# Kernel optimization log

Hardware: AMD Instinct MI355X
Metric: run time of the kernel (lower is better)

## Reference

```python
import jax, jax.numpy as jnp
import numpy as np
import math

B, T, C = 8, 1024, 1024
H = 16
D = C // H
TI = 256
FF = 4 * C
EPS = 1e-5


def _ln(x, g, b):
    mu = jnp.mean(x, axis=-1, keepdims=True)
    var = jnp.mean(jnp.square(x - mu), axis=-1, keepdims=True)
    return (x - mu) * jax.lax.rsqrt(var + EPS) * g + b


def _gelu_tanh(x):
    return jax.nn.gelu(x, approximate=True)


def setup_inputs() -> dict:
    key = jax.random.key(0)
    ks = jax.random.split(key, 16)
    s = 0.02
    inp = {
        'x': jax.random.normal(ks[0], (B, T, C), jnp.float32),
        'x_img_feats': jax.random.normal(ks[1], (B, TI, C), jnp.float32),
        'ln1_g': jnp.ones((C,), jnp.float32), 'ln1_b': jnp.zeros((C,), jnp.float32),
        'ln2_g': jnp.ones((C,), jnp.float32), 'ln2_b': jnp.zeros((C,), jnp.float32),
        'W_attn': jax.random.normal(ks[2], (C, 3 * C), jnp.float32) * s,
        'b_attn': jnp.zeros((3 * C,), jnp.float32),
        'W_aproj': jax.random.normal(ks[3], (C, C), jnp.float32) * s,
        'b_aproj': jnp.zeros((C,), jnp.float32),
        'Wq': jax.random.normal(ks[4], (C, C), jnp.float32) * s,
        'bq': jnp.zeros((C,), jnp.float32),
        'Wk': jax.random.normal(ks[5], (C, C), jnp.float32) * s,
        'bk': jnp.zeros((C,), jnp.float32),
        'Wv': jax.random.normal(ks[6], (C, C), jnp.float32) * s,
        'bv': jnp.zeros((C,), jnp.float32),
        'Wcproj': jax.random.normal(ks[7], (C, C), jnp.float32) * s,
        'bcproj': jnp.zeros((C,), jnp.float32),
        'W_fc': jax.random.normal(ks[8], (C, FF), jnp.float32) * s,
        'b_fc': jnp.zeros((FF,), jnp.float32),
        'W_mproj': jax.random.normal(ks[9], (FF, C), jnp.float32) * s,
        'b_mproj': jnp.zeros((C,), jnp.float32),
    }
    return inp


def _heads(t):
    # (B, S, C) -> (B, H, S, D)
    return t.reshape(t.shape[0], t.shape[1], H, D).transpose(0, 2, 1, 3)


def _merge(t):
    # (B, H, S, D) -> (B, S, C)
    return t.transpose(0, 2, 1, 3).reshape(t.shape[0], t.shape[2], C)


def reference(x, x_img_feats, ln1_g, ln1_b, ln2_g, ln2_b,
              W_attn, b_attn, W_aproj, b_aproj,
              Wq, bq, Wk, bk, Wv, bv, Wcproj, bcproj,
              W_fc, b_fc, W_mproj, b_mproj):
    scale = 1.0 / math.sqrt(D)

    # causal self-attention
    h = _ln(x, ln1_g, ln1_b)
    qkv = h @ W_attn + b_attn
    q, k, v = jnp.split(qkv, 3, axis=-1)
    q, k, v = _heads(q), _heads(k), _heads(v)
    att = jnp.einsum('bhtd,bhsd->bhts', q, k) * scale
    causal = jnp.tril(jnp.ones((T, T), bool))
    att = jnp.where(causal[None, None], att, -jnp.inf)
    att = jax.nn.softmax(att, axis=-1)
    sa = _merge(jnp.einsum('bhts,bhsd->bhtd', att, v)) @ W_aproj + b_aproj
    x = x + sa

    # cross-attention (text queries, image keys/values)
    ht = _ln(x, ln1_g, ln1_b)
    q = _heads(ht @ Wq + bq)
    k = _heads(x_img_feats @ Wk + bk)
    v = _heads(x_img_feats @ Wv + bv)
    catt = jax.nn.softmax(jnp.einsum('bhtd,bhsd->bhts', q, k) * scale, axis=-1)
    ca = _merge(jnp.einsum('bhts,bhsd->bhtd', catt, v)) @ Wcproj + bcproj
    x = x + ca

    # MLP
    h2 = _ln(x, ln2_g, ln2_b)
    x = x + _gelu_tanh(h2 @ W_fc + b_fc) @ W_mproj + b_mproj
    return x
```

## Files before the change

kernel.cpp:

```cpp
#include <hip/hip_runtime.h>

#define B_ 8
#define T_ 1024
#define C_ 1024
#define H_ 16
#define D_ 64
#define TI_ 256
#define FF_ 4096
#define BT_ (B_*T_)
#define BTI_ (B_*TI_)

typedef __bf16 bf16x8 __attribute__((ext_vector_type(8)));
typedef float f32x4 __attribute__((ext_vector_type(4)));

__device__ __forceinline__ unsigned short f2bf(float f){
  unsigned u = __float_as_uint(f);
  u += 0x7fffu + ((u>>16)&1u);
  return (unsigned short)(u>>16);
}

__device__ __forceinline__ void cp16(const void* g, void* l){
  __builtin_amdgcn_global_load_lds(
      (const __attribute__((address_space(1))) unsigned int*)(unsigned long long)g,
      (__attribute__((address_space(3))) unsigned int*)(unsigned long long)l,
      16, 0, 0);
}

__global__ __launch_bounds__(256) void gemm_bt(
    const unsigned short* __restrict__ A,
    const unsigned short* __restrict__ Bt,
    const float* __restrict__ bias,
    const float* __restrict__ resid,
    void* __restrict__ outp,
    int M, int N, int K, int mode)
{
  __shared__ unsigned short sA[128*64];
  __shared__ unsigned short sB[128*64];
  const int tid  = threadIdx.x;
  const int wid  = tid >> 6;
  const int lane = tid & 63;
  const int quad = lane >> 4;
  const int l16  = lane & 15;
  const int row0 = blockIdx.y * 128;
  const int col0 = blockIdx.x * 128;
  const int wr = (wid >> 1) * 64;
  const int wc = (wid & 1) * 64;

  f32x4 zero = {0.f,0.f,0.f,0.f};
  f32x4 acc[4][4];
#pragma unroll
  for (int i=0;i<4;i++)
#pragma unroll
    for (int j=0;j<4;j++) acc[i][j] = zero;

  for (int k0 = 0; k0 < K; k0 += 64){
    if (k0) __syncthreads();
#pragma unroll
    for (int r=0;r<8;r++){
      int chunk = wid*8 + r;
      int cA = chunk & 15;
      int slot = cA*64 + lane;
      int row = slot >> 3;
      int cc = (slot & 7) ^ (row & 7);
      if (chunk < 16)
        cp16(A  + (size_t)(row0+row)*K + (k0 + cc*8), sA + cA*512);
      else
        cp16(Bt + (size_t)(col0+row)*K + (k0 + cc*8), sB + cA*512);
    }
    __syncthreads();
    const char* sAb = (const char*)sA;
    const char* sBb = (const char*)sB;
#pragma unroll
    for (int kk=0;kk<2;kk++){
      bf16x8 af[4], bfb[4];
#pragma unroll
      for (int i=0;i<4;i++){
        int rr = wr + i*16 + l16;
        af[i] = *(const bf16x8*)(sAb + rr*128 + (((kk*4+quad) ^ (rr&7))<<4));
      }
#pragma unroll
      for (int j=0;j<4;j++){
        int rr = wc + j*16 + l16;
        bfb[j] = *(const bf16x8*)(sBb + rr*128 + (((kk*4+quad) ^ (rr&7))<<4));
      }
#pragma unroll
      for (int i=0;i<4;i++)
#pragma unroll
        for (int j=0;j<4;j++)
          acc[i][j] = __builtin_amdgcn_mfma_f32_16x16x32_bf16(af[i], bfb[j], acc[i][j], 0, 0, 0);
    }
  }

#pragma unroll
  for (int j=0;j<4;j++){
    int gc = col0 + wc + j*16 + l16;
    float bz = bias[gc];
#pragma unroll
    for (int i=0;i<4;i++){
      int gr0 = row0 + wr + i*16 + quad*4;
#pragma unroll
      for (int r=0;r<4;r++){
        float v = acc[i][j][r] + bz;
        size_t idx = (size_t)(gr0+r)*N + gc;
        if (mode == 0){
          ((unsigned short*)outp)[idx] = f2bf(v);
        } else if (mode == 1){
          float t = tanhf(0.7978845608028654f*(v + 0.044715f*v*v*v));
          ((unsigned short*)outp)[idx] = f2bf(0.5f*v*(1.f+t));
        } else {
          ((float*)outp)[idx] = resid[idx] + v;
        }
      }
    }
  }
}

__global__ __launch_bounds__(256) void ln_fwd(
    const float* __restrict__ x, const float* __restrict__ g,
    const float* __restrict__ b, unsigned short* __restrict__ out)
{
  int row = blockIdx.x, t = threadIdx.x;
  const float4* xv = (const float4*)(x + (size_t)row*C_);
  float4 v = xv[t];
  float s  = v.x+v.y+v.z+v.w;
  float ss = v.x*v.x + v.y*v.y + v.z*v.z + v.w*v.w;
#pragma unroll
  for (int o=32;o>0;o>>=1){ s += __shfl_down(s,o); ss += __shfl_down(ss,o); }
  __shared__ float red[16];
  int wid = t>>6, lane = t&63;
  if (lane==0){ red[wid]=s; red[8+wid]=ss; }
  __syncthreads();
  if (t==0){
    red[0] = red[0]+red[1]+red[2]+red[3];
    red[8] = red[8]+red[9]+red[10]+red[11];
  }
  __syncthreads();
  float mu  = red[0] * (1.f/C_);
  float var = red[8] * (1.f/C_) - mu*mu;
  float rstd = rsqrtf(var + 1e-5f);
  float4 gv = ((const float4*)g)[t];
  float4 bv = ((const float4*)b)[t];
  ushort4 o;
  o.x = f2bf((v.x-mu)*rstd*gv.x + bv.x);
  o.y = f2bf((v.y-mu)*rstd*gv.y + bv.y);
  o.z = f2bf((v.z-mu)*rstd*gv.z + bv.z);
  o.w = f2bf((v.w-mu)*rstd*gv.w + bv.w);
  ((ushort4*)(out + (size_t)row*C_))[t] = o;
}

__global__ void wconv_t(const float* __restrict__ W, unsigned short* __restrict__ Wt,
                        int Kd, int Nd)
{
  __shared__ float tile[32][33];
  int tx = threadIdx.x, ty = threadIdx.y;
  int n0 = blockIdx.x*32, k0 = blockIdx.y*32;
#pragma unroll
  for (int j=0;j<4;j++)
    tile[ty+8*j][tx] = W[(size_t)(k0+ty+8*j)*Nd + (n0+tx)];
  __syncthreads();
#pragma unroll
  for (int j=0;j<4;j++)
    Wt[(size_t)(n0+ty+8*j)*Kd + (k0+tx)] = f2bf(tile[tx][ty+8*j]);
}

__global__ void conv_bf16(const float* __restrict__ X, unsigned short* __restrict__ Y, int n4)
{
  int i = blockIdx.x*256 + threadIdx.x;
  if (i < n4){
    float4 v = ((const float4*)X)[i];
    ushort4 o; o.x=f2bf(v.x); o.y=f2bf(v.y); o.z=f2bf(v.z); o.w=f2bf(v.w);
    ((ushort4*)Y)[i] = o;
  }
}

__global__ __launch_bounds__(256) void attn_fwd(
    const unsigned short* __restrict__ Q, int ldq,
    const unsigned short* __restrict__ Kp, const unsigned short* __restrict__ Vp, int ldkv,
    int kvT, int Skv, int Tq, int causal,
    unsigned short* __restrict__ Out, int ldo, float scale)
{
  __shared__ unsigned short sK[64*64];
  __shared__ unsigned short sV[64*64];
  __shared__ unsigned short sP[4*16*64];
  const int tid = threadIdx.x;
  const int wid = tid >> 6;
  const int lane = tid & 63;
  const int quad = lane >> 4;
  const int l16 = lane & 15;
  const int qt = blockIdx.x, h = blockIdx.y, b = blockIdx.z;
  const int hoff = h * D_;

  const int qrow = qt*64 + wid*16 + l16;
  const unsigned short* qb = Q + (size_t)(b*Tq + qrow)*ldq + hoff;
  bf16x8 qf[2];
  qf[0] = *(const bf16x8*)(qb + quad*8);
  qf[1] = *(const bf16x8*)(qb + 32 + quad*8);

  f32x4 zero = {0.f,0.f,0.f,0.f};
  f32x4 O[4];
#pragma unroll
  for (int j=0;j<4;j++) O[j] = zero;
  float mrun[4], lrun[4];
#pragma unroll
  for (int r=0;r<4;r++){ mrun[r] = -1e30f; lrun[r] = 0.f; }

  const int nkb = causal ? (qt+1) : ((Skv+63)>>6);
  char* sPw = (char*)sP + wid*2048;

  for (int kb=0; kb<nkb; ++kb){
    if (kb) __syncthreads();
#pragma unroll
    for (int ss=0; ss<2; ++ss){
      int slot = tid + ss*256;
      int srow = slot >> 3;
      int cc = (slot & 7) ^ (srow & 7);
      const unsigned short* g = Kp + (size_t)(b*kvT + kb*64 + srow)*ldkv + hoff + cc*8;
      *(uint4*)((char*)sK + slot*16) = *(const uint4*)g;
    }
    {
      int s_ = lane;
      int dbase = wid*16;
      const unsigned short* gv = Vp + (size_t)(b*kvT + kb*64 + s_)*ldkv + hoff + dbase;
      unsigned short vals[16];
      *(uint4*)(vals)   = *(const uint4*)(gv);
      *(uint4*)(vals+8) = *(const uint4*)(gv+8);
      int chunk = s_ >> 3;
      int sb = (s_ & 7)*2;
#pragma unroll
      for (int jj=0; jj<16; ++jj){
        int d = dbase + jj;
        *(unsigned short*)((char*)sV + d*128 + ((chunk ^ (d&7))<<4) + sb) = vals[jj];
      }
    }
    __syncthreads();

    f32x4 sacc[4];
#pragma unroll
    for (int j=0;j<4;j++) sacc[j] = zero;
#pragma unroll
    for (int j=0;j<4;j++){
      int krow = j*16 + l16;
#pragma unroll
      for (int kk=0;kk<2;kk++){
        bf16x8 kf = *(const bf16x8*)((const char*)sK + krow*128 + (((kk*4+quad) ^ (krow&7))<<4));
        sacc[j] = __builtin_amdgcn_mfma_f32_16x16x32_bf16(qf[kk], kf, sacc[j], 0, 0, 0);
      }
    }
    const int qa0 = qt*64 + wid*16 + quad*4;
    float sc[4][4];
#pragma unroll
    for (int j=0;j<4;j++){
      int key = kb*64 + j*16 + l16;
#pragma unroll
      for (int r=0;r<4;r++){
        float v = sacc[j][r] * scale;
        if (causal && key > qa0 + r) v = -1e30f;
        sc[j][r] = v;
      }
    }
    float mnew[4], alpha[4], rs[4];
#pragma unroll
    for (int r=0;r<4;r++){
      float m = fmaxf(fmaxf(sc[0][r], sc[1][r]), fmaxf(sc[2][r], sc[3][r]));
#pragma unroll
      for (int msk=1; msk<16; msk<<=1) m = fmaxf(m, __shfl_xor(m, msk));
      mnew[r] = fmaxf(mrun[r], m);
      alpha[r] = __expf(mrun[r] - mnew[r]);
      mrun[r] = mnew[r];
      rs[r] = 0.f;
    }
#pragma unroll
    for (int j=0;j<4;j++){
#pragma unroll
      for (int r=0;r<4;r++){
        float p = __expf(sc[j][r] - mnew[r]);
        rs[r] += p;
        int prow = quad*4 + r;
        int cole = j*16 + l16;
        *(unsigned short*)(sPw + prow*128 + (((cole>>3) ^ (prow&7))<<4) + (cole&7)*2) = f2bf(p);
      }
    }
#pragma unroll
    for (int r=0;r<4;r++){
#pragma unroll
      for (int msk=1; msk<16; msk<<=1) rs[r] += __shfl_xor(rs[r], msk);
      lrun[r] = lrun[r]*alpha[r] + rs[r];
    }
#pragma unroll
    for (int j=0;j<4;j++){
      O[j][0] *= alpha[0]; O[j][1] *= alpha[1];
      O[j][2] *= alpha[2]; O[j][3] *= alpha[3];
    }
    bf16x8 pf[2];
#pragma unroll
    for (int kk=0;kk<2;kk++)
      pf[kk] = *(const bf16x8*)(sPw + l16*128 + (((kk*4+quad) ^ (l16&7))<<4));
#pragma unroll
    for (int j=0;j<4;j++){
      int vrow = j*16 + l16;
#pragma unroll
      for (int kk=0;kk<2;kk++){
        bf16x8 vf = *(const bf16x8*)((const char*)sV + vrow*128 + (((kk*4+quad) ^ (vrow&7))<<4));
        O[j] = __builtin_amdgcn_mfma_f32_16x16x32_bf16(pf[kk], vf, O[j], 0, 0, 0);
      }
    }
  }
#pragma unroll
  for (int j=0;j<4;j++){
#pragma unroll
    for (int r=0;r<4;r++){
      int qa = qt*64 + wid*16 + quad*4 + r;
      float o = O[j][r] / lrun[r];
      Out[(size_t)(b*Tq + qa)*ldo + hoff + j*16 + l16] = f2bf(o);
    }
  }
}

extern "C" void kernel_launch(void* const* d_in, const int* in_sizes, int n_in,
                              void* d_out, int out_size, void* d_ws, size_t ws_size,
                              hipStream_t stream)
{
  const float* x       = (const float*)d_in[0];
  const float* ximg    = (const float*)d_in[1];
  const float* ln1_g   = (const float*)d_in[2];
  const float* ln1_b   = (const float*)d_in[3];
  const float* ln2_g   = (const float*)d_in[4];
  const float* ln2_b   = (const float*)d_in[5];
  const float* W_attn  = (const float*)d_in[6];
  const float* b_attn  = (const float*)d_in[7];
  const float* W_aproj = (const float*)d_in[8];
  const float* b_aproj = (const float*)d_in[9];
  const float* Wq = (const float*)d_in[10];
  const float* bq = (const float*)d_in[11];
  const float* Wk = (const float*)d_in[12];
  const float* bk = (const float*)d_in[13];
  const float* Wv = (const float*)d_in[14];
  const float* bv = (const float*)d_in[15];
  const float* Wcproj  = (const float*)d_in[16];
  const float* bcproj  = (const float*)d_in[17];
  const float* W_fc    = (const float*)d_in[18];
  const float* b_fc    = (const float*)d_in[19];
  const float* W_mproj = (const float*)d_in[20];
  const float* b_mproj = (const float*)d_in[21];

  char* ws = (char*)d_ws;
  unsigned short* wt_attn  = (unsigned short*)(ws + 0);
  unsigned short* wt_aproj = (unsigned short*)(ws + 6291456);
  unsigned short* wt_q     = (unsigned short*)(ws + 8388608);
  unsigned short* wt_k     = (unsigned short*)(ws + 10485760);
  unsigned short* wt_v     = (unsigned short*)(ws + 12582912);
  unsigned short* wt_cproj = (unsigned short*)(ws + 14680064);
  unsigned short* wt_fc    = (unsigned short*)(ws + 16777216);
  unsigned short* wt_mproj = (unsigned short*)(ws + 25165824);
  unsigned short* ximg_bf  = (unsigned short*)(ws + 33554432);
  float*          xcur     = (float*)(ws + 37748736);
  unsigned short* h_bf     = (unsigned short*)(ws + 71303168);
  unsigned short* qkv      = (unsigned short*)(ws + 88080384);
  unsigned short* att_out  = (unsigned short*)(ws + 88080384 + 50331648);
  unsigned short* u_bf     = (unsigned short*)(ws + 88080384);
  unsigned short* q2 = (unsigned short*)(ws + 155189248);
  unsigned short* k2 = (unsigned short*)(ws + 171966464);
  unsigned short* v2 = (unsigned short*)(ws + 176160768);
  unsigned short* ca = (unsigned short*)(ws + 180355072);

  dim3 tb(32,8);
  wconv_t<<<dim3(96,32),  tb, 0, stream>>>(W_attn,  wt_attn,  1024, 3072);
  wconv_t<<<dim3(32,32),  tb, 0, stream>>>(W_aproj, wt_aproj, 1024, 1024);
  wconv_t<<<dim3(32,32),  tb, 0, stream>>>(Wq,      wt_q,     1024, 1024);
  wconv_t<<<dim3(32,32),  tb, 0, stream>>>(Wk,      wt_k,     1024, 1024);
  wconv_t<<<dim3(32,32),  tb, 0, stream>>>(Wv,      wt_v,     1024, 1024);
  wconv_t<<<dim3(32,32),  tb, 0, stream>>>(Wcproj,  wt_cproj, 1024, 1024);
  wconv_t<<<dim3(128,32), tb, 0, stream>>>(W_fc,    wt_fc,    1024, 4096);
  wconv_t<<<dim3(32,128), tb, 0, stream>>>(W_mproj, wt_mproj, 4096, 1024);
  conv_bf16<<<BTI_*C_/4/256, 256, 0, stream>>>(ximg, ximg_bf, BTI_*C_/4);
  hipMemcpyAsync(xcur, x, (size_t)BT_*C_*4, hipMemcpyDeviceToDevice, stream);

  ln_fwd<<<BT_, 256, 0, stream>>>(x, ln1_g, ln1_b, h_bf);
  gemm_bt<<<dim3(24,64), 256, 0, stream>>>(h_bf, wt_attn, b_attn, nullptr, qkv, BT_, 3072, 1024, 0);
  attn_fwd<<<dim3(16,H_,B_), 256, 0, stream>>>(qkv, 3072, qkv+1024, qkv+2048, 3072,
                                               T_, T_, T_, 1, att_out, C_, 0.125f);
  gemm_bt<<<dim3(8,64), 256, 0, stream>>>(att_out, wt_aproj, b_aproj, xcur, xcur, BT_, 1024, 1024, 2);

  ln_fwd<<<BT_, 256, 0, stream>>>(xcur, ln1_g, ln1_b, h_bf);
  gemm_bt<<<dim3(8,64), 256, 0, stream>>>(h_bf, wt_q, bq, nullptr, q2, BT_, 1024, 1024, 0);
  gemm_bt<<<dim3(8,16), 256, 0, stream>>>(ximg_bf, wt_k, bk, nullptr, k2, BTI_, 1024, 1024, 0);
  gemm_bt<<<dim3(8,16), 256, 0, stream>>>(ximg_bf, wt_v, bv, nullptr, v2, BTI_, 1024, 1024, 0);
  attn_fwd<<<dim3(16,H_,B_), 256, 0, stream>>>(q2, 1024, k2, v2, 1024,
                                               TI_, TI_, T_, 0, ca, C_, 0.125f);
  gemm_bt<<<dim3(8,64), 256, 0, stream>>>(ca, wt_cproj, bcproj, xcur, xcur, BT_, 1024, 1024, 2);

  ln_fwd<<<BT_, 256, 0, stream>>>(xcur, ln2_g, ln2_b, h_bf);
  gemm_bt<<<dim3(32,64), 256, 0, stream>>>(h_bf, wt_fc, b_fc, nullptr, u_bf, BT_, 4096, 1024, 1);
  gemm_bt<<<dim3(8,64), 256, 0, stream>>>(u_bf, wt_mproj, b_mproj, xcur, (float*)d_out, BT_, 1024, 4096, 2);
}
```

Measured before the change: 832.7 us.

## Use 32x32 MFMA tiles, swizzle block order, fuse K/V projections, sigmoid-form GELU

The GEMM kernel switches from 16x16x32 to 32x32x16 bf16 MFMA with 2x2 accumulator tiles per wave and a matching output index mapping. Blocks are remapped in groups of eight so neighbouring workgroups land in different groups, likely to spread work across XCDs/L2. The K and V projections of the image features become one GEMM with N=2048, relying on wt_k and wt_v being contiguous and on a concatenated bias buffer. The tanh GELU is rewritten as an algebraically equivalent x*sigmoid(2u) using __expf, which is cheaper but slightly less exact.

```diff
diff --git a/kernel.cpp b/kernel.cpp
--- a/kernel.cpp
+++ b/kernel.cpp
@@ -12,6 +12,7 @@
 
 typedef __bf16 bf16x8 __attribute__((ext_vector_type(8)));
 typedef float f32x4 __attribute__((ext_vector_type(4)));
+typedef float f32x16 __attribute__((ext_vector_type(16)));
 
 __device__ __forceinline__ unsigned short f2bf(float f){
   unsigned u = __float_as_uint(f);
@@ -39,19 +40,29 @@
   const int tid  = threadIdx.x;
   const int wid  = tid >> 6;
   const int lane = tid & 63;
-  const int quad = lane >> 4;
-  const int l16  = lane & 15;
-  const int row0 = blockIdx.y * 128;
-  const int col0 = blockIdx.x * 128;
+  const int l32  = lane & 31;
+  const int khalf = lane >> 5;
+
+  int lin = blockIdx.y * gridDim.x + blockIdx.x;
+  int nb  = gridDim.x * gridDim.y;
+  if ((nb & 7) == 0){
+    int per = nb >> 3;
+    lin = (lin >> 3) + (lin & 7) * per;
+  }
+  const int bx = lin % gridDim.x;
+  const int by = lin / gridDim.x;
+  const int row0 = by * 128;
+  const int col0 = bx * 128;
   const int wr = (wid >> 1) * 64;
   const int wc = (wid & 1) * 64;
 
-  f32x4 zero = {0.f,0.f,0.f,0.f};
-  f32x4 acc[4][4];
-#pragma unroll
-  for (int i=0;i<4;i++)
-#pragma unroll
-    for (int j=0;j<4;j++) acc[i][j] = zero;
+  f32x16 acc[2][2];
+#pragma unroll
+  for (int i=0;i<2;i++)
+#pragma unroll
+    for (int j=0;j<2;j++)
+#pragma unroll
+      for (int r=0;r<16;r++) acc[i][j][r] = 0.f;
 
   for (int k0 = 0; k0 < K; k0 += 64){
     if (k0) __syncthreads();
@@ -71,42 +82,44 @@
     const char* sAb = (const char*)sA;
     const char* sBb = (const char*)sB;
 #pragma unroll
-    for (int kk=0;kk<2;kk++){
-      bf16x8 af[4], bfb[4];
-#pragma unroll
-      for (int i=0;i<4;i++){
-        int rr = wr + i*16 + l16;
-        af[i] = *(const bf16x8*)(sAb + rr*128 + (((kk*4+quad) ^ (rr&7))<<4));
-      }
-#pragma unroll
-      for (int j=0;j<4;j++){
-        int rr = wc + j*16 + l16;
-        bfb[j] = *(const bf16x8*)(sBb + rr*128 + (((kk*4+quad) ^ (rr&7))<<4));
-      }
-#pragma unroll
-      for (int i=0;i<4;i++)
-#pragma unroll
-        for (int j=0;j<4;j++)
-          acc[i][j] = __builtin_amdgcn_mfma_f32_16x16x32_bf16(af[i], bfb[j], acc[i][j], 0, 0, 0);
-    }
-  }
-
-#pragma unroll
-  for (int j=0;j<4;j++){
-    int gc = col0 + wc + j*16 + l16;
+    for (int kk=0;kk<4;kk++){
+      bf16x8 af[2], bfb[2];
+#pragma unroll
+      for (int i=0;i<2;i++){
+        int rr = wr + i*32 + l32;
+        af[i] = *(const bf16x8*)(sAb + rr*128 + ((((kk<<1)+khalf) ^ (rr&7))<<4));
+      }
+#pragma unroll
+      for (int j=0;j<2;j++){
+        int rr = wc + j*32 + l32;
+        bfb[j] = *(const bf16x8*)(sBb + rr*128 + ((((kk<<1)+khalf) ^ (rr&7))<<4));
+      }
+#pragma unroll
+      for (int i=0;i<2;i++)
+#pragma unroll
+        for (int j=0;j<2;j++)
+          acc[i][j] = __builtin_amdgcn_mfma_f32_32x32x16_bf16(af[i], bfb[j], acc[i][j], 0, 0, 0);
+    }
+  }
+
+#pragma unroll
+  for (int j=0;j<2;j++){
+    int gc = col0 + wc + j*32 + l32;
     float bz = bias[gc];
 #pragma unroll
-    for (int i=0;i<4;i++){
-      int gr0 = row0 + wr + i*16 + quad*4;
-#pragma unroll
-      for (int r=0;r<4;r++){
-        float v = acc[i][j][r] + bz;
-        size_t idx = (size_t)(gr0+r)*N + gc;
+    for (int i=0;i<2;i++){
+      int gr_base = row0 + wr + i*32 + 4*khalf;
+#pragma unroll
+      for (int reg=0; reg<16; ++reg){
+        int gr = gr_base + (reg&3) + 8*(reg>>2);
+        float v = acc[i][j][reg] + bz;
+        size_t idx = (size_t)gr*N + gc;
         if (mode == 0){
           ((unsigned short*)outp)[idx] = f2bf(v);
         } else if (mode == 1){
-          float t = tanhf(0.7978845608028654f*(v + 0.044715f*v*v*v));
-          ((unsigned short*)outp)[idx] = f2bf(0.5f*v*(1.f+t));
+          float w = 1.5957691216057308f*(v + 0.044715f*v*v*v);
+          float g = v / (1.f + __expf(-w));
+          ((unsigned short*)outp)[idx] = f2bf(g);
         } else {
           ((float*)outp)[idx] = resid[idx] + v;
         }
@@ -358,10 +371,10 @@
   unsigned short* qkv      = (unsigned short*)(ws + 88080384);
   unsigned short* att_out  = (unsigned short*)(ws + 88080384 + 50331648);
   unsigned short* u_bf     = (unsigned short*)(ws + 88080384);
-  unsigned short* q2 = (unsigned short*)(ws + 155189248);
-  unsigned short* k2 = (unsigned short*)(ws + 171966464);
-  unsigned short* v2 = (unsigned short*)(ws + 176160768);
-  unsigned short* ca = (unsigned short*)(ws + 180355072);
+  unsigned short* q2   = (unsigned short*)(ws + 155189248);
+  unsigned short* k2v2 = (unsigned short*)(ws + 171966464);
+  unsigned short* ca   = (unsigned short*)(ws + 180355072);
+  float*          bkv  = (float*)(ws + 197132288);
 
   dim3 tb(32,8);
   wconv_t<<<dim3(96,32),  tb, 0, stream>>>(W_attn,  wt_attn,  1024, 3072);
@@ -374,6 +387,8 @@
   wconv_t<<<dim3(32,128), tb, 0, stream>>>(W_mproj, wt_mproj, 4096, 1024);
   conv_bf16<<<BTI_*C_/4/256, 256, 0, stream>>>(ximg, ximg_bf, BTI_*C_/4);
   hipMemcpyAsync(xcur, x, (size_t)BT_*C_*4, hipMemcpyDeviceToDevice, stream);
+  hipMemcpyAsync(bkv,        bk, 4096, hipMemcpyDeviceToDevice, stream);
+  hipMemcpyAsync(bkv + 1024, bv, 4096, hipMemcpyDeviceToDevice, stream);
 
   ln_fwd<<<BT_, 256, 0, stream>>>(x, ln1_g, ln1_b, h_bf);
   gemm_bt<<<dim3(24,64), 256, 0, stream>>>(h_bf, wt_attn, b_attn, nullptr, qkv, BT_, 3072, 1024, 0);
@@ -383,9 +398,8 @@
 
   ln_fwd<<<BT_, 256, 0, stream>>>(xcur, ln1_g, ln1_b, h_bf);
   gemm_bt<<<dim3(8,64), 256, 0, stream>>>(h_bf, wt_q, bq, nullptr, q2, BT_, 1024, 1024, 0);
-  gemm_bt<<<dim3(8,16), 256, 0, stream>>>(ximg_bf, wt_k, bk, nullptr, k2, BTI_, 1024, 1024, 0);
-  gemm_bt<<<dim3(8,16), 256, 0, stream>>>(ximg_bf, wt_v, bv, nullptr, v2, BTI_, 1024, 1024, 0);
-  attn_fwd<<<dim3(16,H_,B_), 256, 0, stream>>>(q2, 1024, k2, v2, 1024,
+  gemm_bt<<<dim3(16,16), 256, 0, stream>>>(ximg_bf, wt_k, bkv, nullptr, k2v2, BTI_, 2048, 1024, 0);
+  attn_fwd<<<dim3(16,H_,B_), 256, 0, stream>>>(q2, 1024, k2v2, k2v2+1024, 2048,
                                                TI_, TI_, T_, 0, ca, C_, 0.125f);
   gemm_bt<<<dim3(8,64), 256, 0, stream>>>(ca, wt_cproj, bcproj, xcur, xcur, BT_, 1024, 1024, 2);
 
```

New measurement: 839.2 us. No clear change (+0.8%).
